# Optimization experiments

Measured on AMD Instinct MI355X. Metric: run time of the kernel, lower is better.

The kernel has to match this reference:

```python
import jax, jax.numpy as jnp
import numpy as np

N = 100_000   # nodes
E = 1_600_000 # edges
K = 3         # Chebyshev order


def _cheb_norm(row, col, w, n):
    # PyG ChebConv norm with normalization='sym', lambda_max=2:
    # L_hat = 2L/lambda_max - I = -D^{-1/2} A D^{-1/2} (diagonal cancels),
    # so only the off-diagonal term survives.
    deg = jax.ops.segment_sum(w, row, num_segments=n)
    dis = jnp.where(deg > 0, jax.lax.rsqrt(deg), 0.0)
    return -dis[row] * w * dis[col]


def _propagate(x, row, col, norm, n):
    # y[i] = sum_{e: row[e]=i} norm[e] * x[col[e]]   (sparse matvec with L_hat)
    return jax.ops.segment_sum(norm[:, None] * x[col], row, num_segments=n)


def _cheb_conv(x, row, col, norm, W, b, n):
    # Chebyshev recursion: T0=x, T1=L_hat x, T_k = 2 L_hat T_{k-1} - T_{k-2}
    Tx0 = x
    out = Tx0 @ W[0]
    Tx1 = _propagate(Tx0, row, col, norm, n)
    out = out + Tx1 @ W[1]
    for k in range(2, W.shape[0]):
        Tx2 = 2.0 * _propagate(Tx1, row, col, norm, n) - Tx0
        out = out + Tx2 @ W[k]
        Tx0, Tx1 = Tx1, Tx2
    return out + b


def setup_inputs() -> dict:
    key = jax.random.key(0)
    ks = jax.random.split(key, 8)
    in_f, c1, c2, out_f = 50, 64, 64, 16
    return {
        "x": jax.random.normal(ks[0], (N, in_f), jnp.float32),
        "edge_index": jax.random.randint(ks[1], (2, E), 0, N),
        "edge_weight": jax.random.uniform(ks[2], (E,), jnp.float32),
        "W1": jax.random.normal(ks[3], (K, in_f, c1), jnp.float32) * 0.05,
        "b1": jnp.zeros((c1,), jnp.float32),
        "W2": jax.random.normal(ks[4], (K, c1, c2), jnp.float32) * 0.05,
        "b2": jnp.zeros((c2,), jnp.float32),
        "bn_gamma": jnp.ones((c1,), jnp.float32),
        "bn_beta": jnp.zeros((c1,), jnp.float32),
        "lin_W": jax.random.normal(ks[5], (out_f, c2), jnp.float32) * 0.05,
        "lin_b": jnp.zeros((out_f,), jnp.float32),
    }


def reference(x, edge_index, edge_weight, W1, b1, W2, b2, bn_gamma, bn_beta, lin_W, lin_b):
    row, col = edge_index[0], edge_index[1]
    n = x.shape[0]
    norm = _cheb_norm(row, col, edge_weight, n)
    # conv1 + relu
    h = jax.nn.relu(_cheb_conv(x, row, col, norm, W1, b1, n))
    # BatchNorm1d over the node dimension (training-mode batch stats, eps=1e-5)
    mu = h.mean(axis=0)
    var = h.var(axis=0)
    h = (h - mu) * jax.lax.rsqrt(var + 1e-5) * bn_gamma + bn_beta
    # dropout with p=0.0 -> identity
    h = jax.nn.relu(_cheb_conv(h, row, col, norm, W2, b2, n))
    return h @ lin_W.T + lin_b
```

## Files before the change

kernel.cpp:

```cpp
#include <hip/hip_runtime.h>
#include <hip/hip_bf16.h>
#include <hip/hip_fp16.h>

static constexpr int NF   = 50;
static constexpr int C1   = 64;
static constexpr int OUTF = 16;
static constexpr int SCAN_T = 256;
static constexpr int SCAN_I = 4;
static constexpr float DEG_SCALE   = 8388608.f;
static constexpr float DEG_INV     = 1.f / 8388608.f;

typedef _Float16 half8 __attribute__((ext_vector_type(8)));
typedef float    f32x4 __attribute__((ext_vector_type(4)));

__global__ void pass1_kernel(const int* __restrict__ row, const float* __restrict__ w,
                             unsigned long long* __restrict__ pcd, int* __restrict__ rank, int e)
{
    int i = blockIdx.x * blockDim.x + threadIdx.x;
    if (i < e) {
        int r = row[i];
        unsigned int wq = (unsigned int)(w[i] * DEG_SCALE + 0.5f);
        unsigned long long pk = (1ULL << 32) | (unsigned long long)wq;
        unsigned long long old = atomicAdd(&pcd[r], pk);
        rank[i] = (int)(old >> 32);
    }
}

__global__ void dis_kernel(const unsigned long long* __restrict__ pcd,
                           float* __restrict__ dis, int* __restrict__ cnt, int n)
{
    int i = blockIdx.x * blockDim.x + threadIdx.x;
    if (i < n) {
        unsigned long long pk = pcd[i];
        int c = (int)(pk >> 32);
        float d = (float)(unsigned int)(pk & 0xFFFFFFFFu) * DEG_INV;
        cnt[i] = c;
        dis[i] = (d > 0.f) ? (1.f / sqrtf(d)) : 0.f;
    }
}

__global__ void scan_partial(const int* __restrict__ cnt, int* __restrict__ bsum, int n)
{
    __shared__ int sm[SCAN_T];
    int t = threadIdx.x;
    int base = blockIdx.x * SCAN_T * SCAN_I + t * SCAN_I;
    int s = 0;
    #pragma unroll
    for (int k = 0; k < SCAN_I; ++k) { int i = base + k; if (i < n) s += cnt[i]; }
    sm[t] = s; __syncthreads();
    for (int off = SCAN_T / 2; off > 0; off >>= 1) {
        if (t < off) sm[t] += sm[t + off];
        __syncthreads();
    }
    if (t == 0) bsum[blockIdx.x] = sm[0];
}

__global__ void scan_bsums(int* __restrict__ bsum, int nb)
{
    __shared__ int sm[256];
    int t = threadIdx.x;
    sm[t] = (t < nb) ? bsum[t] : 0;
    __syncthreads();
    for (int off = 1; off < 256; off <<= 1) {
        int v = (t >= off) ? sm[t - off] : 0;
        __syncthreads();
        sm[t] += v;
        __syncthreads();
    }
    if (t < nb) bsum[t] = (t == 0) ? 0 : sm[t - 1];
}

__global__ void scan_final(const int* __restrict__ cnt, const int* __restrict__ bsum,
                           int* __restrict__ rowptr, int n)
{
    __shared__ int sm[SCAN_T];
    int t = threadIdx.x;
    int base = blockIdx.x * SCAN_T * SCAN_I + t * SCAN_I;
    int v[SCAN_I]; int s = 0;
    #pragma unroll
    for (int k = 0; k < SCAN_I; ++k) { int i = base + k; v[k] = (i < n) ? cnt[i] : 0; s += v[k]; }
    sm[t] = s; __syncthreads();
    for (int off = 1; off < SCAN_T; off <<= 1) {
        int x = (t >= off) ? sm[t - off] : 0;
        __syncthreads();
        sm[t] += x;
        __syncthreads();
    }
    int pref = bsum[blockIdx.x] + sm[t] - s;
    #pragma unroll
    for (int k = 0; k < SCAN_I; ++k) {
        int i = base + k;
        if (i < n) { rowptr[i] = pref; pref += v[k]; }
    }
}

__global__ void scatter_kernel(const int* __restrict__ row, const int* __restrict__ col,
                               const float* __restrict__ w, const float* __restrict__ dis,
                               const int* __restrict__ rowptr, const int* __restrict__ rank,
                               int2* __restrict__ ecn, int e)
{
    int i = blockIdx.x * blockDim.x + threadIdx.x;
    if (i < e) {
        int r = row[i], c = col[i];
        int pos = rowptr[r] + rank[i];
        float nv = -dis[r] * w[i] * dis[c];
        ecn[pos] = make_int2(c, __float_as_int(nv));
    }
}

__global__ void padx_kernel(const float* __restrict__ x, __half* __restrict__ XH, int n64)
{
    int i = blockIdx.x * blockDim.x + threadIdx.x;
    if (i < n64) {
        int row = i >> 6, f = i & 63;
        XH[i] = __float2half((f < NF) ? x[row * NF + f] : 0.f);
    }
}

__global__ void wprep_kernel(const float* __restrict__ W2, __half* __restrict__ WTh)
{
    int i = blockIdx.x * blockDim.x + threadIdx.x;
    if (i < 3 * C1 * C1) {
        int tap = i / (C1 * C1), rem = i % (C1 * C1), col = rem / C1, k = rem % C1;
        WTh[i] = __float2half(W2[tap * C1 * C1 + k * C1 + col]);
    }
}

template<int BS, bool SHADOW>
__global__ __launch_bounds__(256) void prop_kernel(
    const __half* __restrict__ xin, const float* __restrict__ base,
    const int* __restrict__ rowptr, const int* __restrict__ cnt,
    const int2* __restrict__ ecn, float* __restrict__ yout,
    __half* __restrict__ ysh, int n)
{
    int gw = (blockIdx.x * blockDim.x + threadIdx.x) >> 6;
    int lane = threadIdx.x & 63;
    if (gw >= n) return;
    int st = __builtin_amdgcn_readfirstlane(rowptr[gw]);
    int m  = __builtin_amdgcn_readfirstlane(cnt[gw]);
    float a[8] = {0.f, 0.f, 0.f, 0.f, 0.f, 0.f, 0.f, 0.f};
    for (int t = 0; t < m; t += 8) {
        #pragma unroll
        for (int k = 0; k < 8; ++k) {
            int tk = t + k;
            int idx = st + min(tk, m - 1);
            int2 md = ecn[idx];
            float nv = (tk < m) ? __int_as_float(md.y) : 0.f;
            a[k] += nv * __half2float(xin[md.x * C1 + lane]);
        }
    }
    float acc = ((a[0] + a[1]) + (a[2] + a[3])) + ((a[4] + a[5]) + (a[6] + a[7]));
    if (BS > 0) {
        float bv = (BS == C1 || lane < BS) ? base[(size_t)gw * BS + lane] : 0.f;
        acc = 2.f * acc - bv;
    }
    yout[(size_t)gw * C1 + lane] = acc;
    if (SHADOW) ysh[(size_t)gw * C1 + lane] = __float2half(acc);
}

__global__ __launch_bounds__(512) void dense1_kernel(
    const float* __restrict__ x, float* U , const float* __restrict__ T2,
    const float* __restrict__ W1, const float* __restrict__ b1,
    float* __restrict__ stats, int n)
{
    __shared__ __align__(16) float WI[3 * 13 * 64 * 4];
    __shared__ __align__(16) float ROWS[8 * 4 * 3 * 64];
    __shared__ float red[2][8][64];
    const int tid = threadIdx.x;
    for (int i = tid; i < 3 * 13 * 64 * 4; i += 512) WI[i] = 0.f;
    __syncthreads();
    for (int i = tid; i < 3 * NF * C1; i += 512) {
        int tap = i / (NF * C1), rem = i % (NF * C1), f = rem / C1, j = rem % C1;
        WI[((tap * 13 + (f >> 2)) * 64 + j) * 4 + (f & 3)] = W1[i];
    }
    __syncthreads();

    const int lane = tid & 63;
    const int wv   = tid >> 6;
    const int gw   = blockIdx.x * 8 + wv;
    const int rstep = gridDim.x * 8 * 4;
    const float bias = b1[lane];
    const float4* W4 = (const float4*)WI;
    const float4* R4 = (const float4*)ROWS;
    float ssum = 0.f, ssq = 0.f;

    for (int r0 = gw * 4; r0 < n; r0 += rstep) {
        const int nr = min(4, n - r0);
        #pragma unroll
        for (int r = 0; r < 4; ++r) {
            int row = min(r0 + r, n - 1);
            ROWS[((wv * 4 + r) * 3 + 0) * 64 + lane] = (lane < NF) ? x[row * NF + lane] : 0.f;
            ROWS[((wv * 4 + r) * 3 + 1) * 64 + lane] = U [row * C1 + lane];
            ROWS[((wv * 4 + r) * 3 + 2) * 64 + lane] = T2[row * C1 + lane];
        }
        float acc[4] = {bias, bias, bias, bias};
        for (int c = 0; c < 13; ++c) {
            float4 w0 = W4[(0 * 13 + c) * 64 + lane];
            float4 w1 = W4[(1 * 13 + c) * 64 + lane];
            float4 w2 = W4[(2 * 13 + c) * 64 + lane];
            #pragma unroll
            for (int r = 0; r < 4; ++r) {
                float4 t0 = R4[((wv * 4 + r) * 3 + 0) * 16 + c];
                float4 t1 = R4[((wv * 4 + r) * 3 + 1) * 16 + c];
                float4 t2 = R4[((wv * 4 + r) * 3 + 2) * 16 + c];
                acc[r] += t0.x * w0.x + t0.y * w0.y + t0.z * w0.z + t0.w * w0.w
                        + t1.x * w1.x + t1.y * w1.y + t1.z * w1.z + t1.w * w1.w
                        + t2.x * w2.x + t2.y * w2.y + t2.z * w2.z + t2.w * w2.w;
            }
        }
        #pragma unroll
        for (int r = 0; r < 4; ++r) {
            if (r < nr) {
                float v = fmaxf(acc[r], 0.f);
                U[(r0 + r) * C1 + lane] = v;
                ssum += v; ssq += v * v;
            }
        }
    }
    red[0][wv][lane] = ssum;
    red[1][wv][lane] = ssq;
    __syncthreads();
    if (tid < 128) {
        int which = tid >> 6, j = tid & 63;
        float tot = 0.f;
        #pragma unroll
        for (int wq = 0; wq < 8; ++wq) tot += red[which][wq][j];
        atomicAdd(&stats[which * 64 + j], tot);
    }
}

__global__ void bn_finalize_kernel(float* __restrict__ stats, const float* __restrict__ gamma,
                                   const float* __restrict__ beta, float inv_n)
{
    int j = threadIdx.x;
    if (j < 64) {
        float mu   = stats[j] * inv_n;
        float var  = stats[64 + j] * inv_n - mu * mu;
        float rstd = 1.f / sqrtf(var + 1e-5f);
        float sc   = gamma[j] * rstd;
        stats[128 + j] = sc;
        stats[192 + j] = beta[j] - mu * sc;
    }
}

__global__ void bn_apply_kernel(float* __restrict__ h, __half2* __restrict__ hh,
                                const float* __restrict__ stats, int n4)
{
    int i = blockIdx.x * blockDim.x + threadIdx.x;
    const int stride = gridDim.x * blockDim.x;
    int j0 = (i * 4) & 63;
    float s0 = stats[128 + j0], s1 = stats[129 + j0], s2 = stats[130 + j0], s3 = stats[131 + j0];
    float b0 = stats[192 + j0], b1 = stats[193 + j0], b2 = stats[194 + j0], b3 = stats[195 + j0];
    float4* h4 = (float4*)h;
    for (; i < n4; i += stride) {
        float4 v = h4[i];
        v.x = v.x * s0 + b0;
        v.y = v.y * s1 + b1;
        v.z = v.z * s2 + b2;
        v.w = v.w * s3 + b3;
        h4[i] = v;
        hh[i * 2 + 0] = __floats2half2_rn(v.x, v.y);
        hh[i * 2 + 1] = __floats2half2_rn(v.z, v.w);
    }
}

__global__ __launch_bounds__(512) void dense2_kernel(
    const __half* __restrict__ hb16, const __half* __restrict__ q16,
    const __half* __restrict__ t16,  const __half* __restrict__ WTh,
    const float* __restrict__ b2, const float* __restrict__ linW,
    const float* __restrict__ linb, float* __restrict__ out, int n)
{
    __shared__ float LWT[C1 * OUTF];
    __shared__ float gst[8][16][65];
    const int tid = threadIdx.x;
    for (int i = tid; i < C1 * OUTF; i += 512) {
        int j = i / OUTF, o = i % OUTF;
        LWT[i] = linW[o * C1 + j];
    }
    __syncthreads();

    const int lane = tid & 63, wv = tid >> 6;
    const int cl = lane & 15, rg = lane >> 4;
    const int nt = n >> 4;
    const float lb = linb[cl];

    for (int tile = blockIdx.x * 8 + wv; tile < nt; tile += gridDim.x * 8) {
        int r0 = tile * 16;
        const __half* ta = hb16 + (size_t)(r0 + cl) * C1 + rg * 8;
        const __half* tb = q16  + (size_t)(r0 + cl) * C1 + rg * 8;
        const __half* tc = t16  + (size_t)(r0 + cl) * C1 + rg * 8;
        half8 a00 = *(const half8*)(ta);   half8 a01 = *(const half8*)(ta + 32);
        half8 a10 = *(const half8*)(tb);   half8 a11 = *(const half8*)(tb + 32);
        half8 a20 = *(const half8*)(tc);   half8 a21 = *(const half8*)(tc + 32);

        #pragma unroll
        for (int ct = 0; ct < 4; ++ct) {
            float bias = b2[ct * 16 + cl];
            f32x4 acc = {bias, bias, bias, bias};
            const __half* wb = WTh + (ct * 16 + cl) * C1 + rg * 8;
            acc = __builtin_amdgcn_mfma_f32_16x16x32_f16(a00, *(const half8*)(wb),              acc, 0, 0, 0);
            acc = __builtin_amdgcn_mfma_f32_16x16x32_f16(a01, *(const half8*)(wb + 32),         acc, 0, 0, 0);
            acc = __builtin_amdgcn_mfma_f32_16x16x32_f16(a10, *(const half8*)(wb + 4096),       acc, 0, 0, 0);
            acc = __builtin_amdgcn_mfma_f32_16x16x32_f16(a11, *(const half8*)(wb + 4096 + 32),  acc, 0, 0, 0);
            acc = __builtin_amdgcn_mfma_f32_16x16x32_f16(a20, *(const half8*)(wb + 8192),       acc, 0, 0, 0);
            acc = __builtin_amdgcn_mfma_f32_16x16x32_f16(a21, *(const half8*)(wb + 8192 + 32),  acc, 0, 0, 0);
            #pragma unroll
            for (int r = 0; r < 4; ++r)
                gst[wv][rg * 4 + r][ct * 16 + cl] = fmaxf(acc[r], 0.f);
        }
        #pragma unroll
        for (int r4 = 0; r4 < 4; ++r4) {
            int row = r4 * 4 + rg;
            float oa = lb;
            #pragma unroll 8
            for (int j = 0; j < C1; ++j)
                oa += gst[wv][row][j] * LWT[j * OUTF + cl];
            out[(size_t)(r0 + row) * OUTF + cl] = oa;
        }
    }
}

extern "C" void kernel_launch(void* const* d_in, const int* in_sizes, int n_in,
                              void* d_out, int out_size, void* d_ws, size_t ws_size,
                              hipStream_t stream)
{
    const float* x     = (const float*)d_in[0];
    const int*   ei    = (const int*)  d_in[1];
    const float* ew    = (const float*)d_in[2];
    const float* W1    = (const float*)d_in[3];
    const float* b1    = (const float*)d_in[4];
    const float* W2    = (const float*)d_in[5];
    const float* b2    = (const float*)d_in[6];
    const float* gamma = (const float*)d_in[7];
    const float* beta  = (const float*)d_in[8];
    const float* linW  = (const float*)d_in[9];
    const float* linb  = (const float*)d_in[10];
    float* out = (float*)d_out;
    (void)n_in; (void)out_size; (void)ws_size;

    const int n = in_sizes[0] / NF;
    const int e = in_sizes[2];
    const int* row = ei;
    const int* col = ei + e;

    char* ws = (char*)d_ws;
    size_t off = 0;
    auto alloc = [&](size_t bytes) -> void* {
        void* p = ws + off;
        off += (bytes + 255) & ~(size_t)255;
        return p;
    };
    unsigned long long* pcd = (unsigned long long*)alloc((size_t)n * 8);
    float*  dis    = (float*)alloc((size_t)n * 4);
    int*    cnt    = (int*)  alloc((size_t)n * 4);
    int*    rowptr = (int*)  alloc((size_t)n * 4);
    int*    rank   = (int*)  alloc((size_t)e * 4);
    int*    bsum   = (int*)  alloc(256 * 4);
    float*  stats  = (float*)alloc(256 * 4);
    int2*   ecn    = (int2*) alloc((size_t)e * 8);
    __half* XH     = (__half*)alloc((size_t)n * C1 * 2);
    __half* T1H    = (__half*)alloc((size_t)n * C1 * 2);
    __half* HH     = (__half*)alloc((size_t)n * C1 * 2);
    __half* Q1H    = (__half*)alloc((size_t)n * C1 * 2);
    __half* SH     = (__half*)alloc((size_t)n * C1 * 2);
    __half* WTh    = (__half*)alloc((size_t)3 * C1 * C1 * 2);
    float*  U      = (float*)alloc((size_t)n * C1 * 4);
    float*  H      = (float*)alloc((size_t)n * C1 * 4);
    float*  S      = (float*)alloc((size_t)n * C1 * 4);

    hipMemsetAsync(pcd,   0, (size_t)n * 8, stream);
    hipMemsetAsync(stats, 0, 256 * 4, stream);

    const int eb  = (e + 255) / 256;
    const int nbk = (n + 255) / 256;
    pass1_kernel<<<eb, 256, 0, stream>>>(row, ew, pcd, rank, e);
    dis_kernel<<<nbk, 256, 0, stream>>>(pcd, dis, cnt, n);
    padx_kernel<<<(n * C1 + 255) / 256, 256, 0, stream>>>(x, XH, n * C1);
    wprep_kernel<<<(3 * C1 * C1 + 255) / 256, 256, 0, stream>>>(W2, WTh);

    const int nb = (n + SCAN_T * SCAN_I - 1) / (SCAN_T * SCAN_I);
    scan_partial<<<nb, SCAN_T, 0, stream>>>(cnt, bsum, n);
    scan_bsums<<<1, 256, 0, stream>>>(bsum, nb);
    scan_final<<<nb, SCAN_T, 0, stream>>>(cnt, bsum, rowptr, n);
    scatter_kernel<<<eb, 256, 0, stream>>>(row, col, ew, dis, rowptr, rank, ecn, e);

    const int pb = (n + 3) / 4;

    prop_kernel<0,  true ><<<pb, 256, 0, stream>>>(XH,  x, rowptr, cnt, ecn, U, T1H, n);
    prop_kernel<NF, false><<<pb, 256, 0, stream>>>(T1H, x, rowptr, cnt, ecn, H, T1H, n);
    dense1_kernel<<<1024, 512, 0, stream>>>(x, U, H, W1, b1, stats, n);
    bn_finalize_kernel<<<1, 64, 0, stream>>>(stats, gamma, beta, 1.f / (float)n);
    bn_apply_kernel<<<2048, 256, 0, stream>>>(U, (__half2*)HH, stats, n * C1 / 4);

    prop_kernel<0,  true ><<<pb, 256, 0, stream>>>(HH,  U, rowptr, cnt, ecn, H, Q1H, n);
    prop_kernel<C1, true ><<<pb, 256, 0, stream>>>(Q1H, U, rowptr, cnt, ecn, S, SH, n);
    dense2_kernel<<<512, 512, 0, stream>>>(HH, Q1H, SH, WTh, b2, linW, linb, out, n);
}
```

Measured before the change: 475.8 us.

## Rewrite layer-one dense transform with fp16 MFMA on half-precision shadow inputs

The first-layer dense combine of x, T1 and T2 with W1 now uses 16x16x32 fp16 MFMA instructions instead of scalar FP32 FMAs from shared memory. It reads fp16 copies of the three inputs, so the second propagation also writes an fp16 shadow of T2 and a new kernel pre-transposes W1 into padded fp16. This cuts the FP32 read traffic and the scalar compute of the dense stage, at the cost of fp16 rounding on inputs and weights. The tile loop handles only full 16-row tiles, which works for n=100000 but leaves tail rows unwritten for other sizes.

```diff
diff --git a/kernel.cpp b/kernel.cpp
--- a/kernel.cpp
+++ b/kernel.cpp
@@ -126,6 +126,15 @@
     }
 }
 
+__global__ void wprep1_kernel(const float* __restrict__ W1, __half* __restrict__ WTh1)
+{
+    int i = blockIdx.x * blockDim.x + threadIdx.x;
+    if (i < 3 * C1 * C1) {
+        int tap = i / (C1 * C1), rem = i % (C1 * C1), col = rem / C1, k = rem % C1;
+        WTh1[i] = __float2half((k < NF) ? W1[(tap * NF + k) * C1 + col] : 0.f);
+    }
+}
+
 template<int BS, bool SHADOW>
 __global__ __launch_bounds__(256) void prop_kernel(
     const __half* __restrict__ xin, const float* __restrict__ base,
@@ -159,66 +168,62 @@
 }
 
 __global__ __launch_bounds__(512) void dense1_kernel(
-    const float* __restrict__ x, float* U , const float* __restrict__ T2,
-    const float* __restrict__ W1, const float* __restrict__ b1,
+    const __half* __restrict__ xh, const __half* __restrict__ t1h,
+    const __half* __restrict__ t2h, const __half* __restrict__ WTh1,
+    const float* __restrict__ b1, float* __restrict__ U,
     float* __restrict__ stats, int n)
 {
-    __shared__ __align__(16) float WI[3 * 13 * 64 * 4];
-    __shared__ __align__(16) float ROWS[8 * 4 * 3 * 64];
+    __shared__ float gst[8][16][65];
     __shared__ float red[2][8][64];
     const int tid = threadIdx.x;
-    for (int i = tid; i < 3 * 13 * 64 * 4; i += 512) WI[i] = 0.f;
-    __syncthreads();
-    for (int i = tid; i < 3 * NF * C1; i += 512) {
-        int tap = i / (NF * C1), rem = i % (NF * C1), f = rem / C1, j = rem % C1;
-        WI[((tap * 13 + (f >> 2)) * 64 + j) * 4 + (f & 3)] = W1[i];
-    }
-    __syncthreads();
-
-    const int lane = tid & 63;
-    const int wv   = tid >> 6;
-    const int gw   = blockIdx.x * 8 + wv;
-    const int rstep = gridDim.x * 8 * 4;
-    const float bias = b1[lane];
-    const float4* W4 = (const float4*)WI;
-    const float4* R4 = (const float4*)ROWS;
-    float ssum = 0.f, ssq = 0.f;
-
-    for (int r0 = gw * 4; r0 < n; r0 += rstep) {
-        const int nr = min(4, n - r0);
-        #pragma unroll
-        for (int r = 0; r < 4; ++r) {
-            int row = min(r0 + r, n - 1);
-            ROWS[((wv * 4 + r) * 3 + 0) * 64 + lane] = (lane < NF) ? x[row * NF + lane] : 0.f;
-            ROWS[((wv * 4 + r) * 3 + 1) * 64 + lane] = U [row * C1 + lane];
-            ROWS[((wv * 4 + r) * 3 + 2) * 64 + lane] = T2[row * C1 + lane];
-        }
-        float acc[4] = {bias, bias, bias, bias};
-        for (int c = 0; c < 13; ++c) {
-            float4 w0 = W4[(0 * 13 + c) * 64 + lane];
-            float4 w1 = W4[(1 * 13 + c) * 64 + lane];
-            float4 w2 = W4[(2 * 13 + c) * 64 + lane];
+    const int lane = tid & 63, wv = tid >> 6;
+    const int cl = lane & 15, rg = lane >> 4;
+    const int nt = n >> 4;
+    float ssum[4] = {0.f, 0.f, 0.f, 0.f}, ssq[4] = {0.f, 0.f, 0.f, 0.f};
+
+    for (int tile = blockIdx.x * 8 + wv; tile < nt; tile += gridDim.x * 8) {
+        int r0 = tile * 16;
+        const __half* ta = xh  + (size_t)(r0 + cl) * C1 + rg * 8;
+        const __half* tb = t1h + (size_t)(r0 + cl) * C1 + rg * 8;
+        const __half* tc = t2h + (size_t)(r0 + cl) * C1 + rg * 8;
+        half8 a00 = *(const half8*)(ta);   half8 a01 = *(const half8*)(ta + 32);
+        half8 a10 = *(const half8*)(tb);   half8 a11 = *(const half8*)(tb + 32);
+        half8 a20 = *(const half8*)(tc);   half8 a21 = *(const half8*)(tc + 32);
+
+        #pragma unroll
+        for (int ct = 0; ct < 4; ++ct) {
+            float bias = b1[ct * 16 + cl];
+            f32x4 acc = {bias, bias, bias, bias};
+            const __half* wb = WTh1 + (ct * 16 + cl) * C1 + rg * 8;
+            acc = __builtin_amdgcn_mfma_f32_16x16x32_f16(a00, *(const half8*)(wb),             acc, 0, 0, 0);
+            acc = __builtin_amdgcn_mfma_f32_16x16x32_f16(a01, *(const half8*)(wb + 32),        acc, 0, 0, 0);
+            acc = __builtin_amdgcn_mfma_f32_16x16x32_f16(a10, *(const half8*)(wb + 4096),      acc, 0, 0, 0);
+            acc = __builtin_amdgcn_mfma_f32_16x16x32_f16(a11, *(const half8*)(wb + 4096 + 32), acc, 0, 0, 0);
+            acc = __builtin_amdgcn_mfma_f32_16x16x32_f16(a20, *(const half8*)(wb + 8192),      acc, 0, 0, 0);
+            acc = __builtin_amdgcn_mfma_f32_16x16x32_f16(a21, *(const half8*)(wb + 8192 + 32), acc, 0, 0, 0);
             #pragma unroll
             for (int r = 0; r < 4; ++r) {
-                float4 t0 = R4[((wv * 4 + r) * 3 + 0) * 16 + c];
-                float4 t1 = R4[((wv * 4 + r) * 3 + 1) * 16 + c];
-                float4 t2 = R4[((wv * 4 + r) * 3 + 2) * 16 + c];
-                acc[r] += t0.x * w0.x + t0.y * w0.y + t0.z * w0.z + t0.w * w0.w
-                        + t1.x * w1.x + t1.y * w1.y + t1.z * w1.z + t1.w * w1.w
-                        + t2.x * w2.x + t2.y * w2.y + t2.z * w2.z + t2.w * w2.w;
+                float v = fmaxf(acc[r], 0.f);
+                gst[wv][rg * 4 + r][ct * 16 + cl] = v;
+                ssum[ct] += v; ssq[ct] += v * v;
             }
         }
         #pragma unroll
-        for (int r = 0; r < 4; ++r) {
-            if (r < nr) {
-                float v = fmaxf(acc[r], 0.f);
-                U[(r0 + r) * C1 + lane] = v;
-                ssum += v; ssq += v * v;
-            }
+        for (int row = 0; row < 16; ++row)
+            U[(size_t)(r0 + row) * C1 + lane] = gst[wv][row][lane];
+    }
+    #pragma unroll
+    for (int ct = 0; ct < 4; ++ct) {
+        ssum[ct] += __shfl_xor(ssum[ct], 16); ssum[ct] += __shfl_xor(ssum[ct], 32);
+        ssq[ct]  += __shfl_xor(ssq[ct], 16);  ssq[ct]  += __shfl_xor(ssq[ct], 32);
+    }
+    if (rg == 0) {
+        #pragma unroll
+        for (int ct = 0; ct < 4; ++ct) {
+            red[0][wv][ct * 16 + cl] = ssum[ct];
+            red[1][wv][ct * 16 + cl] = ssq[ct];
         }
     }
-    red[0][wv][lane] = ssum;
-    red[1][wv][lane] = ssq;
     __syncthreads();
     if (tid < 128) {
         int which = tid >> 6, j = tid & 63;
@@ -360,10 +365,12 @@
     int2*   ecn    = (int2*) alloc((size_t)e * 8);
     __half* XH     = (__half*)alloc((size_t)n * C1 * 2);
     __half* T1H    = (__half*)alloc((size_t)n * C1 * 2);
+    __half* T2H    = (__half*)alloc((size_t)n * C1 * 2);
     __half* HH     = (__half*)alloc((size_t)n * C1 * 2);
     __half* Q1H    = (__half*)alloc((size_t)n * C1 * 2);
     __half* SH     = (__half*)alloc((size_t)n * C1 * 2);
     __half* WTh    = (__half*)alloc((size_t)3 * C1 * C1 * 2);
+    __half* WTh1   = (__half*)alloc((size_t)3 * C1 * C1 * 2);
     float*  U      = (float*)alloc((size_t)n * C1 * 4);
     float*  H      = (float*)alloc((size_t)n * C1 * 4);
     float*  S      = (float*)alloc((size_t)n * C1 * 4);
@@ -377,6 +384,7 @@
     dis_kernel<<<nbk, 256, 0, stream>>>(pcd, dis, cnt, n);
     padx_kernel<<<(n * C1 + 255) / 256, 256, 0, stream>>>(x, XH, n * C1);
     wprep_kernel<<<(3 * C1 * C1 + 255) / 256, 256, 0, stream>>>(W2, WTh);
+    wprep1_kernel<<<(3 * C1 * C1 + 255) / 256, 256, 0, stream>>>(W1, WTh1);
 
     const int nb = (n + SCAN_T * SCAN_I - 1) / (SCAN_T * SCAN_I);
     scan_partial<<<nb, SCAN_T, 0, stream>>>(cnt, bsum, n);
@@ -387,8 +395,8 @@
     const int pb = (n + 3) / 4;
 
     prop_kernel<0,  true ><<<pb, 256, 0, stream>>>(XH,  x, rowptr, cnt, ecn, U, T1H, n);
-    prop_kernel<NF, false><<<pb, 256, 0, stream>>>(T1H, x, rowptr, cnt, ecn, H, T1H, n);
-    dense1_kernel<<<1024, 512, 0, stream>>>(x, U, H, W1, b1, stats, n);
+    prop_kernel<NF, true ><<<pb, 256, 0, stream>>>(T1H, x, rowptr, cnt, ecn, H, T2H, n);
+    dense1_kernel<<<512, 512, 0, stream>>>(XH, T1H, T2H, WTh1, b1, U, stats, n);
     bn_finalize_kernel<<<1, 64, 0, stream>>>(stats, gamma, beta, 1.f / (float)n);
     bn_apply_kernel<<<2048, 256, 0, stream>>>(U, (__half2*)HH, stats, n * C1 / 4);
 
```

Result: faster. 440.9 us (-7.3%).
